# Performance work log

Measured on AMD Instinct MI355X. Metric: run time of the kernel, lower is better.

Reference implementation:

```python
import jax, jax.numpy as jnp
import numpy as np

BINS = 10
NUM_CLASSES = 2


def setup_inputs() -> dict:
    key = jax.random.key(0)
    k1, k2 = jax.random.split(key)
    N = 16777216
    pred = jax.random.uniform(k1, (N, NUM_CLASSES), dtype=jnp.float32)
    target = jax.random.randint(k2, (N,), 0, NUM_CLASSES, dtype=jnp.int64)
    return {"pred": pred, "target": target}


def reference(pred, target):
    N = pred.shape[0]
    # one-hot target, gradient magnitude (detached in torch -> stop_gradient)
    one_hot = jax.nn.one_hot(target, NUM_CLASSES, dtype=pred.dtype)
    g = jnp.abs(jax.lax.stop_gradient(pred) - one_hot)  # [N, 2]

    edges = jnp.arange(BINS + 1, dtype=jnp.float32) / BINS
    edges = edges.at[-1].add(1e-6)

    # bin index: i such that edges[i] <= g < edges[i+1]
    idx = jnp.searchsorted(edges, g, side="right") - 1  # [N, 2]
    valid = (idx >= 0) & (idx < BINS)
    idx_c = jnp.clip(idx, 0, BINS - 1)

    # histogram of valid gradients (single pass, replaces per-bin mask loop)
    counts = jax.ops.segment_sum(
        valid.astype(jnp.float32).ravel(), idx_c.ravel(), num_segments=BINS
    )  # [BINS]
    n_nonempty = jnp.sum(counts > 0).astype(pred.dtype)

    # momentum == 0 path: weight = tot / num_in_bin for non-empty bins
    cnt_per_elem = counts[idx_c]  # [N, 2]
    tot = jnp.asarray(N, dtype=pred.dtype)
    weights = jnp.where(valid & (cnt_per_elem > 0), tot / cnt_per_elem, 0.0)
    weights = jnp.where(n_nonempty > 0, weights / n_nonempty, weights)

    # nll_loss(pred, target, reduction='none') = -pred[i, target[i]]
    loss = -jnp.take_along_axis(pred, target[:, None], axis=1)[:, 0]  # [N]
    weighted_loss = jnp.sum(loss * weights.mean(axis=1)) / tot
    return weighted_loss
```

## Files before the change

### kernel.cpp

```cpp
#include <hip/hip_runtime.h>

#define BINS 10
#define NTHREADS 256
#define GRID 2048

#define CNT_SHIFT 25
#define SUM_SCALE 262144.0f
#define SUM_INV   (1.0f / 262144.0f)
#define SUM_MASK  0x01FFFFFFu

__device__ __forceinline__ void do_row(float p0, float p1, int t,
                                       unsigned int* __restrict__ col)
{
    const bool  is0 = (t == 0);
    const float g0  = is0 ? (1.0f - p0) : p0;
    const float g1  = is0 ? p1 : (1.0f - p1);
    const float pt  = is0 ? p0 : p1;
    const int b0 = min((int)(g0 * 10.0f), 9);
    const int b1 = min((int)(g1 * 10.0f), 9);
    const unsigned int inc =
        (1u << CNT_SHIFT) + (unsigned int)__fmaf_rn(pt, SUM_SCALE, 0.5f);
    atomicAdd(&col[b0 * NTHREADS], inc);
    atomicAdd(&col[b1 * NTHREADS], inc);
}

#define DO_GROUP(A, B, C, D, T0, T1)            \
    do {                                        \
        do_row((A).x, (A).y, (T0).x, col);      \
        do_row((A).z, (A).w, (T0).y, col);      \
        do_row((B).x, (B).y, (T0).z, col);      \
        do_row((B).z, (B).w, (T0).w, col);      \
        do_row((C).x, (C).y, (T1).x, col);      \
        do_row((C).z, (C).w, (T1).y, col);      \
        do_row((D).x, (D).y, (T1).z, col);      \
        do_row((D).z, (D).w, (T1).w, col);      \
    } while (0)

__global__ __launch_bounds__(NTHREADS, 8) void ghm_hist_kernel(
    const float* __restrict__ pred,
    const int* __restrict__ target,
    int N,
    int* __restrict__ part_cnt,
    float* __restrict__ part_sum)
{
    __shared__ unsigned int s_hist[BINS][NTHREADS];
    __shared__ int   s_c[4][BINS];
    __shared__ float s_s[4][BINS];

    const int tid = threadIdx.x;
    unsigned int* col = &s_hist[0][tid];

    #pragma unroll
    for (int b = 0; b < BINS; ++b) col[b * NTHREADS] = 0u;

    const int gtid   = blockIdx.x * blockDim.x + tid;
    const int stride = gridDim.x * blockDim.x;
    const int n8     = N >> 3;
    const int iters  = n8 / stride;

    const float4* __restrict__ pred4 = (const float4*)pred;
    const int4*   __restrict__ tgt4  = (const int4*)target;

    for (int k = 0; k < iters; ++k) {
        const int i = gtid + k * stride;
        const float4 A  = pred4[4 * i + 0];
        const float4 B  = pred4[4 * i + 1];
        const float4 C  = pred4[4 * i + 2];
        const float4 D  = pred4[4 * i + 3];
        const int4   t0 = tgt4[2 * i + 0];
        const int4   t1 = tgt4[2 * i + 1];
        DO_GROUP(A, B, C, D, t0, t1);
    }

    {
        const int r = iters * stride + gtid;
        if (r < n8) {
            const float4 A  = pred4[4 * r + 0];
            const float4 B  = pred4[4 * r + 1];
            const float4 C  = pred4[4 * r + 2];
            const float4 D  = pred4[4 * r + 3];
            const int4   t0 = tgt4[2 * r + 0];
            const int4   t1 = tgt4[2 * r + 1];
            DO_GROUP(A, B, C, D, t0, t1);
        }
    }
    {
        const int row = n8 * 8 + gtid;
        if (row < N)
            do_row(pred[2 * row], pred[2 * row + 1], target[row], col);
    }

    __syncthreads();

    int   cnt[BINS];
    float sum[BINS];
    #pragma unroll
    for (int b = 0; b < BINS; ++b) {
        const unsigned int w = col[b * NTHREADS];
        cnt[b] = (int)(w >> CNT_SHIFT);
        sum[b] = (float)(w & SUM_MASK) * SUM_INV;
    }

    const int lane = tid & 63;
    const int wave = tid >> 6;
    #pragma unroll
    for (int b = 0; b < BINS; ++b) {
        int   c = cnt[b];
        float s = sum[b];
        #pragma unroll
        for (int off = 32; off > 0; off >>= 1) {
            c += __shfl_down(c, off);
            s += __shfl_down(s, off);
        }
        if (lane == 0) { s_c[wave][b] = c; s_s[wave][b] = s; }
    }
    __syncthreads();
    if (tid < BINS) {
        const int c = s_c[0][tid] + s_c[1][tid] + s_c[2][tid] + s_c[3][tid];
        const float s = s_s[0][tid] + s_s[1][tid] + s_s[2][tid] + s_s[3][tid];
        part_cnt[tid * GRID + blockIdx.x] = c;
        part_sum[tid * GRID + blockIdx.x] = s;
    }
}

__global__ __launch_bounds__(NTHREADS) void ghm_reduce_kernel(
    const int* __restrict__ part_cnt,
    const float* __restrict__ part_sum,
    float* __restrict__ out)
{
    __shared__ int   s_c[4][BINS];
    __shared__ float s_s[4][BINS];
    const int tid = threadIdx.x;

    int   c[BINS];
    float s[BINS];
    #pragma unroll
    for (int b = 0; b < BINS; ++b) { c[b] = 0; s[b] = 0.0f; }

    for (int e = tid; e < GRID; e += NTHREADS) {
        #pragma unroll
        for (int b = 0; b < BINS; ++b) {
            c[b] += part_cnt[b * GRID + e];
            s[b] += part_sum[b * GRID + e];
        }
    }

    const int lane = tid & 63;
    const int wave = tid >> 6;
    #pragma unroll
    for (int b = 0; b < BINS; ++b) {
        int   cc = c[b];
        float ss = s[b];
        #pragma unroll
        for (int off = 32; off > 0; off >>= 1) {
            cc += __shfl_down(cc, off);
            ss += __shfl_down(ss, off);
        }
        if (lane == 0) { s_c[wave][b] = cc; s_s[wave][b] = ss; }
    }
    __syncthreads();
    if (tid == 0) {
        int nne = 0;
        float acc = 0.0f;
        #pragma unroll
        for (int b = 0; b < BINS; ++b) {
            const int   cc = s_c[0][b] + s_c[1][b] + s_c[2][b] + s_c[3][b];
            const float ss = s_s[0][b] + s_s[1][b] + s_s[2][b] + s_s[3][b];
            if (cc > 0) { nne++; acc += ss / (float)cc; }
        }
        out[0] = (nne > 0) ? (-acc / (2.0f * (float)nne)) : 0.0f;
    }
}

extern "C" void kernel_launch(void* const* d_in, const int* in_sizes, int n_in,
                              void* d_out, int out_size, void* d_ws, size_t ws_size,
                              hipStream_t stream) {
    const float* pred   = (const float*)d_in[0];
    const int*   target = (const int*)d_in[1];
    const int N = in_sizes[1];

    int*   part_cnt = (int*)d_ws;
    float* part_sum = (float*)((char*)d_ws + BINS * GRID * sizeof(int));

    ghm_hist_kernel<<<GRID, NTHREADS, 0, stream>>>(pred, target, N, part_cnt, part_sum);
    ghm_reduce_kernel<<<1, NTHREADS, 0, stream>>>(part_cnt, part_sum, (float*)d_out);
}
```

Before: 48.21 us.

## Software-pipeline histogram loads with 4-row stages and vectorize final reduce

The histogram kernel now handles 4 rows per stage instead of 8 and prefetches the next stage's pred and target vectors before processing the current one, to overlap global-load latency with the shared-memory atomics. The reduce kernel runs with 512 threads and reads partials as int4/float4 in one pass instead of a strided loop. The reduce now assumes GRID/4 equals the thread count. The smaller stage loads fewer bytes per iteration, which may cost some of the memory-level parallelism the prefetch is meant to add.

```diff
diff --git a/kernel.cpp b/kernel.cpp
--- a/kernel.cpp
+++ b/kernel.cpp
@@ -24,16 +24,12 @@
     atomicAdd(&col[b1 * NTHREADS], inc);
 }
 
-#define DO_GROUP(A, B, C, D, T0, T1)            \
+#define DO_STAGE(A, B, T)                       \
     do {                                        \
-        do_row((A).x, (A).y, (T0).x, col);      \
-        do_row((A).z, (A).w, (T0).y, col);      \
-        do_row((B).x, (B).y, (T0).z, col);      \
-        do_row((B).z, (B).w, (T0).w, col);      \
-        do_row((C).x, (C).y, (T1).x, col);      \
-        do_row((C).z, (C).w, (T1).y, col);      \
-        do_row((D).x, (D).y, (T1).z, col);      \
-        do_row((D).z, (D).w, (T1).w, col);      \
+        do_row((A).x, (A).y, (T).x, col);       \
+        do_row((A).z, (A).w, (T).y, col);       \
+        do_row((B).x, (B).y, (T).z, col);       \
+        do_row((B).z, (B).w, (T).w, col);       \
     } while (0)
 
 __global__ __launch_bounds__(NTHREADS, 8) void ghm_hist_kernel(
@@ -55,37 +51,41 @@
 
     const int gtid   = blockIdx.x * blockDim.x + tid;
     const int stride = gridDim.x * blockDim.x;
-    const int n8     = N >> 3;
-    const int iters  = n8 / stride;
+    const int n4     = N >> 2;
+    const int iters  = n4 / stride;
 
     const float4* __restrict__ pred4 = (const float4*)pred;
     const int4*   __restrict__ tgt4  = (const int4*)target;
 
-    for (int k = 0; k < iters; ++k) {
-        const int i = gtid + k * stride;
-        const float4 A  = pred4[4 * i + 0];
-        const float4 B  = pred4[4 * i + 1];
-        const float4 C  = pred4[4 * i + 2];
-        const float4 D  = pred4[4 * i + 3];
-        const int4   t0 = tgt4[2 * i + 0];
-        const int4   t1 = tgt4[2 * i + 1];
-        DO_GROUP(A, B, C, D, t0, t1);
+    float4 cA, cB;
+    int4   cT;
+    int i = gtid;
+    if (iters > 0) {
+        cA = pred4[2 * i + 0];
+        cB = pred4[2 * i + 1];
+        cT = tgt4[i];
     }
+    for (int k = 1; k < iters; ++k) {
+        const int j = i + stride;
+        const float4 nA = pred4[2 * j + 0];
+        const float4 nB = pred4[2 * j + 1];
+        const int4   nT = tgt4[j];
+        DO_STAGE(cA, cB, cT);
+        cA = nA; cB = nB; cT = nT; i = j;
+    }
+    if (iters > 0) DO_STAGE(cA, cB, cT);
 
     {
         const int r = iters * stride + gtid;
-        if (r < n8) {
-            const float4 A  = pred4[4 * r + 0];
-            const float4 B  = pred4[4 * r + 1];
-            const float4 C  = pred4[4 * r + 2];
-            const float4 D  = pred4[4 * r + 3];
-            const int4   t0 = tgt4[2 * r + 0];
-            const int4   t1 = tgt4[2 * r + 1];
-            DO_GROUP(A, B, C, D, t0, t1);
+        if (r < n4) {
+            const float4 A = pred4[2 * r + 0];
+            const float4 B = pred4[2 * r + 1];
+            const int4   T = tgt4[r];
+            DO_STAGE(A, B, T);
         }
     }
     {
-        const int row = n8 * 8 + gtid;
+        const int row = n4 * 4 + gtid;
         if (row < N)
             do_row(pred[2 * row], pred[2 * row + 1], target[row], col);
     }
@@ -116,33 +116,33 @@
     }
     __syncthreads();
     if (tid < BINS) {
-        const int c = s_c[0][tid] + s_c[1][tid] + s_c[2][tid] + s_c[3][tid];
+        const int   c = s_c[0][tid] + s_c[1][tid] + s_c[2][tid] + s_c[3][tid];
         const float s = s_s[0][tid] + s_s[1][tid] + s_s[2][tid] + s_s[3][tid];
         part_cnt[tid * GRID + blockIdx.x] = c;
         part_sum[tid * GRID + blockIdx.x] = s;
     }
 }
 
-__global__ __launch_bounds__(NTHREADS) void ghm_reduce_kernel(
+__global__ __launch_bounds__(512) void ghm_reduce_kernel(
     const int* __restrict__ part_cnt,
     const float* __restrict__ part_sum,
     float* __restrict__ out)
 {
-    __shared__ int   s_c[4][BINS];
-    __shared__ float s_s[4][BINS];
+    __shared__ int   s_c[8][BINS];
+    __shared__ float s_s[8][BINS];
     const int tid = threadIdx.x;
+
+    const int4*   __restrict__ pc4 = (const int4*)part_cnt;
+    const float4* __restrict__ ps4 = (const float4*)part_sum;
 
     int   c[BINS];
     float s[BINS];
     #pragma unroll
-    for (int b = 0; b < BINS; ++b) { c[b] = 0; s[b] = 0.0f; }
-
-    for (int e = tid; e < GRID; e += NTHREADS) {
-        #pragma unroll
-        for (int b = 0; b < BINS; ++b) {
-            c[b] += part_cnt[b * GRID + e];
-            s[b] += part_sum[b * GRID + e];
-        }
+    for (int b = 0; b < BINS; ++b) {
+        const int4   vc = pc4[b * (GRID / 4) + tid];
+        const float4 vs = ps4[b * (GRID / 4) + tid];
+        c[b] = vc.x + vc.y + vc.z + vc.w;
+        s[b] = vs.x + vs.y + vs.z + vs.w;
     }
 
     const int lane = tid & 63;
@@ -164,8 +164,10 @@
         float acc = 0.0f;
         #pragma unroll
         for (int b = 0; b < BINS; ++b) {
-            const int   cc = s_c[0][b] + s_c[1][b] + s_c[2][b] + s_c[3][b];
-            const float ss = s_s[0][b] + s_s[1][b] + s_s[2][b] + s_s[3][b];
+            int   cc = 0;
+            float ss = 0.0f;
+            #pragma unroll
+            for (int w = 0; w < 8; ++w) { cc += s_c[w][b]; ss += s_s[w][b]; }
             if (cc > 0) { nne++; acc += ss / (float)cc; }
         }
         out[0] = (nne > 0) ? (-acc / (2.0f * (float)nne)) : 0.0f;
@@ -183,5 +185,5 @@
     float* part_sum = (float*)((char*)d_ws + BINS * GRID * sizeof(int));
 
     ghm_hist_kernel<<<GRID, NTHREADS, 0, stream>>>(pred, target, N, part_cnt, part_sum);
-    ghm_reduce_kernel<<<1, NTHREADS, 0, stream>>>(part_cnt, part_sum, (float*)d_out);
+    ghm_reduce_kernel<<<1, 512, 0, stream>>>(part_cnt, part_sum, (float*)d_out);
 }
```

Measured after the change: 45.34 us. 1.06x faster.
